# Kernel tuning notes

Hardware: AMD Instinct MI355X
Metric: run time of the kernel (lower is better)

Reference implementation:

```python
import jax, jax.numpy as jnp
import numpy as np
from jax import lax

NH = 8        # num_heads
C = 256       # embedding_dim
WS = 5        # window_size
DN = ('NCHW', 'OIHW', 'NCHW')


def setup_inputs() -> dict:
    key = jax.random.key(0)
    ks = jax.random.split(key, 6)
    B, H, W = 16, 64, 64
    hd = C // NH  # per-head dim = pos_embed_dim
    return {
        "src": jax.random.normal(ks[0], (B, C, H, W), jnp.float32),
        "rel_pos_embed": jax.random.normal(ks[1], (hd, WS, WS), jnp.float32) * 0.02,
        "qkv_w": jax.random.normal(ks[2], (3 * C, C), jnp.float32) * (C ** -0.5),
        "cpe_w": jax.random.normal(ks[3], (C, C, 3, 3), jnp.float32) * (1.0 / np.sqrt(C * 9)),
        "cpe_b": jnp.zeros((C,), jnp.float32),
        "out_w": jax.random.normal(ks[4], (C, C), jnp.float32) * (C ** -0.5),
        "out_b": jnp.zeros((C,), jnp.float32),
    }


def reference(src, rel_pos_embed, qkv_w, cpe_w, cpe_b, out_w, out_b):
    B, Cc, H, W = src.shape
    hd = Cc // NH
    scale = hd ** -0.5

    # conv positional encoding (3x3 conv) + residual
    x = lax.conv_general_dilated(src, cpe_w, (1, 1), [(1, 1), (1, 1)],
                                 dimension_numbers=DN) + cpe_b[None, :, None, None] + src

    # 1x1 qkv conv as a GEMM over channels
    qkv = jnp.einsum('oc,bchw->bohw', qkv_w, x)
    q, k, v = jnp.split(qkv, 3, axis=1)
    q = q.reshape(B * NH, hd, H, W)
    k = k.reshape(B * NH, hd, H, W)
    v = v.reshape(B * NH, hd, H, W)

    # linear (lambda) attention: softmax over spatial positions of k
    kf = jax.nn.softmax(k.reshape(B * NH, hd, H * W), axis=-1)   # (b' i n)
    vf = v.reshape(B * NH, hd, H * W)                            # (b' o n)
    content_lambda = jnp.einsum('bin,bon->bio', kf, vf)          # (b' i o), tiny
    qf = q.reshape(B * NH, hd, H * W) * scale
    content = jnp.einsum('bin,bio->bon', qf, content_lambda).reshape(B * NH, hd, H, W)

    # depthwise conv positional lambda on v
    pad = WS // 2
    pos_lambda = lax.conv_general_dilated(v, rel_pos_embed[:, None], (1, 1),
                                          [(pad, pad), (pad, pad)],
                                          dimension_numbers=DN,
                                          feature_group_count=hd)
    result = (content + q * pos_lambda).reshape(B, Cc, H, W)

    # 1x1 output projection
    return jnp.einsum('oc,bchw->bohw', out_w, result) + out_b[None, :, None, None]
```

## Files before the change

### kernel.cpp

```cpp
#include <hip/hip_runtime.h>


typedef unsigned short u16;
typedef __bf16 bf16x8 __attribute__((ext_vector_type(8)));
typedef float f32x4 __attribute__((ext_vector_type(4)));
#define HW 4096

__device__ __forceinline__ float bf2f(u16 u){
  unsigned v = ((unsigned)u) << 16;
  return __builtin_bit_cast(float, v);
}
__device__ __forceinline__ u16 f2bf(float f){
  unsigned u = __builtin_bit_cast(unsigned, f);
  u = u + 0x7fffu + ((u >> 16) & 1u);
  return (u16)(u >> 16);
}
__device__ __forceinline__ unsigned pack2(float a, float b){
  return (unsigned)f2bf(a) | ((unsigned)f2bf(b) << 16);
}
__device__ __forceinline__ void unpack2(unsigned u, float& a, float& b){
  a = bf2f((u16)(u & 0xffffu)); b = bf2f((u16)(u >> 16));
}
__device__ __forceinline__ void unp8(uint4 r, float* v){
  unpack2(r.x, v[0], v[1]); unpack2(r.y, v[2], v[3]);
  unpack2(r.z, v[4], v[5]); unpack2(r.w, v[6], v[7]);
}

__device__ __forceinline__ void gl2lds16(const u16* g, u16* l){
  __builtin_amdgcn_global_load_lds((__attribute__((address_space(1))) void*)g,
                                   (__attribute__((address_space(3))) void*)l, 16, 0, 0);
}

__global__ void zero_border(u16* __restrict__ xpad){
  int idx = blockIdx.x*256 + threadIdx.x;
  int g = idx & 31;
  int p = idx >> 5;
  int b = p / 260; int r = p - b*260;
  int y, x;
  if (r < 66)      { y = 0;      x = r; }
  else if (r < 132){ y = 65;     x = r-66; }
  else if (r < 196){ y = r-131;  x = 0; }
  else             { y = r-195;  x = 65; }
  *(uint4*)&xpad[((size_t)b*4356 + (size_t)y*66 + x)*256 + g*8] = uint4{0,0,0,0};
}

__global__ __launch_bounds__(256) void to_nhwc(const float* __restrict__ src,
                                               u16* __restrict__ xpad){
  __shared__ u16 sl[64*264];
  const int t = threadIdx.x, w = t>>6, lane = t&63;
  const int y = blockIdx.x, b = blockIdx.y;
  for (int cc = 0; cc < 64; ++cc){
    const int c = cc*4 + w;
    float v = src[((size_t)(b*256 + c))*HW + y*64 + lane];
    sl[lane*264 + c] = f2bf(v);
  }
  __syncthreads();
  #pragma unroll
  for (int i = 0; i < 8; ++i){
    int idx = t + 256*i;
    int p = idx >> 5, g = idx & 31;
    uint4 v = *(const uint4*)&sl[p*264 + g*8];
    *(uint4*)&xpad[((size_t)b*4356 + (size_t)(y+1)*66 + (p+1))*256 + g*8] = v;
  }
}

__global__ void repack_w(const float* __restrict__ cpe_w, const float* __restrict__ qkv_w,
                         const float* __restrict__ out_w, u16* __restrict__ wrb,
                         u16* __restrict__ wq, u16* __restrict__ wo){
  int idx = blockIdx.x*256 + threadIdx.x;
  if (idx < 589824){
    int kk = idx >> 16, o = (idx >> 8) & 255, c = idx & 255;
    wrb[idx] = f2bf(cpe_w[((o*256 + c)*9) + kk]);
  } else if (idx < 786432){
    int j = idx - 589824;
    wq[j] = f2bf(qkv_w[j]);
  } else {
    int j = idx - 786432;
    wo[j] = f2bf(out_w[j]);
  }
}

__global__ __launch_bounds__(256) void conv_mfma(const u16* __restrict__ xpad,
    const u16* __restrict__ wrb, const float* __restrict__ bias,
    u16* __restrict__ xout){
  __shared__ u16 As[8192];
  __shared__ u16 Bs[8192];
  const int t = threadIdx.x, w = t>>6, lane = t&63;
  const int idx = blockIdx.x;
  const int x8 = idx&7, q = idx>>3;
  const int ot = q & 1, nb = (q>>1)*8 + x8;
  const int pg = nb*128;
  const int b = pg>>12, hw0 = pg&4095, y0 = hw0>>6;
  const int o0 = ot*128;
  const size_t xb = (size_t)b*4356;
  const int sp8 = t>>3;
  const int cs8 = (t&7) ^ (sp8&7);
  const u16* aA[4]; const u16* bB[4];
  #pragma unroll
  for (int i = 0; i < 4; ++i){
    aA[i] = xpad + (xb + (size_t)(y0 + (i>>1) + 1)*66 + ((i&1)*32 + sp8) + 1)*256 + cs8*8;
    bB[i] = wrb + (size_t)(o0 + i*32 + sp8)*256 + cs8*8;
  }
  const int wm = w&1, wn = w>>1;
  const int qd = lane>>4;
  int a_off[4], b_off[4];
  #pragma unroll
  for (int i = 0; i < 4; ++i){
    int p = wm*64 + i*16 + (lane&15);
    a_off[i] = p*64 + ((qd ^ (p&7)) << 3);
    int r = wn*64 + i*16 + (lane&15);
    b_off[i] = r*64 + ((qd ^ (r&7)) << 3);
  }
  f32x4 acc[4][4];
  #pragma unroll
  for (int i=0;i<4;++i)
    #pragma unroll
    for (int j=0;j<4;++j) acc[i][j] = f32x4{0.f,0.f,0.f,0.f};

  for (int c0 = 0; c0 < 256; c0 += 64){
    for (int kk = 0; kk < 9; ++kk){
      const int toff = ((kk/3 - 1)*66 + (kk%3 - 1))*256 + c0;
      const int woff = kk*65536 + c0;
      __syncthreads();
      #pragma unroll
      for (int i = 0; i < 4; ++i){
        gl2lds16(aA[i] + toff, &As[i*2048 + t*8]);
        gl2lds16(bB[i] + woff, &Bs[i*2048 + t*8]);
      }
      __syncthreads();
      #pragma unroll
      for (int kh = 0; kh < 2; ++kh){
        bf16x8 af[4], bfr[4];
        #pragma unroll
        for (int i = 0; i < 4; ++i){
          af[i]  = __builtin_bit_cast(bf16x8, *(const uint4*)&As[a_off[i] ^ (kh<<5)]);
          bfr[i] = __builtin_bit_cast(bf16x8, *(const uint4*)&Bs[b_off[i] ^ (kh<<5)]);
        }
        #pragma unroll
        for (int mt = 0; mt < 4; ++mt)
          #pragma unroll
          for (int nt = 0; nt < 4; ++nt)
            acc[mt][nt] = __builtin_amdgcn_mfma_f32_16x16x32_bf16(bfr[nt], af[mt], acc[mt][nt], 0,0,0);
      }
    }
  }
  #pragma unroll
  for (int nt = 0; nt < 4; ++nt){
    const int och4 = o0 + wn*64 + nt*16 + (lane>>4)*4;
    float4 b4 = *(const float4*)&bias[och4];
    #pragma unroll
    for (int mt = 0; mt < 4; ++mt){
      const int px = wm*64 + mt*16 + (lane&15);
      const int hw = hw0 + px;
      const int y = hw>>6, x = hw&63;
      ushort4 r4 = *(const ushort4*)&xpad[(xb + (size_t)(y+1)*66 + x + 1)*256 + och4];
      ushort4 s;
      s.x = f2bf(acc[mt][nt][0] + b4.x + bf2f(r4.x));
      s.y = f2bf(acc[mt][nt][1] + b4.y + bf2f(r4.y));
      s.z = f2bf(acc[mt][nt][2] + b4.z + bf2f(r4.z));
      s.w = f2bf(acc[mt][nt][3] + b4.w + bf2f(r4.w));
      *(ushort4*)&xout[(size_t)(pg + px)*256 + och4] = s;
    }
  }
}

template<int NO, int NOT, bool F32OUT>
__global__ __launch_bounds__(256) void gemm_mfma(const u16* __restrict__ act,
    const u16* __restrict__ wt, const float* __restrict__ bias, void* __restrict__ out){
  __shared__ u16 As[8192];
  __shared__ u16 Bs[8192];
  const int t = threadIdx.x, w = t>>6, lane = t&63;
  const int idx = blockIdx.x;
  const int x8 = idx&7, q = idx>>3;
  const int ot = q % NOT, nb = (q / NOT)*8 + x8;
  const int pg = nb*128, o0 = ot*128;
  const int sp8 = t>>3;
  const int cs8 = (t&7) ^ (sp8&7);
  const u16* aA[4]; const u16* bB[4];
  #pragma unroll
  for (int i = 0; i < 4; ++i){
    aA[i] = act + (size_t)(pg + i*32 + sp8)*256 + cs8*8;
    bB[i] = wt  + (size_t)(o0 + i*32 + sp8)*256 + cs8*8;
  }
  const int wm = w&1, wn = w>>1;
  const int qd = lane>>4;
  int a_off[4], b_off[4];
  #pragma unroll
  for (int i = 0; i < 4; ++i){
    int p = wm*64 + i*16 + (lane&15);
    a_off[i] = p*64 + ((qd ^ (p&7)) << 3);
    int r = wn*64 + i*16 + (lane&15);
    b_off[i] = r*64 + ((qd ^ (r&7)) << 3);
  }
  f32x4 acc[4][4];
  #pragma unroll
  for (int i=0;i<4;++i)
    #pragma unroll
    for (int j=0;j<4;++j) acc[i][j] = f32x4{0.f,0.f,0.f,0.f};

  for (int c0 = 0; c0 < 256; c0 += 64){
    __syncthreads();
    #pragma unroll
    for (int i = 0; i < 4; ++i){
      gl2lds16(aA[i] + c0, &As[i*2048 + t*8]);
      gl2lds16(bB[i] + c0, &Bs[i*2048 + t*8]);
    }
    __syncthreads();
    #pragma unroll
    for (int kh = 0; kh < 2; ++kh){
      bf16x8 af[4], bfr[4];
      #pragma unroll
      for (int i = 0; i < 4; ++i){
        af[i]  = __builtin_bit_cast(bf16x8, *(const uint4*)&As[a_off[i] ^ (kh<<5)]);
        bfr[i] = __builtin_bit_cast(bf16x8, *(const uint4*)&Bs[b_off[i] ^ (kh<<5)]);
      }
      #pragma unroll
      for (int mt = 0; mt < 4; ++mt)
        #pragma unroll
        for (int nt = 0; nt < 4; ++nt){
          if constexpr (F32OUT)
            acc[mt][nt] = __builtin_amdgcn_mfma_f32_16x16x32_bf16(af[mt], bfr[nt], acc[mt][nt], 0,0,0);
          else
            acc[mt][nt] = __builtin_amdgcn_mfma_f32_16x16x32_bf16(bfr[nt], af[mt], acc[mt][nt], 0,0,0);
        }
    }
  }
  if constexpr (F32OUT){
    const int col = lane&15, row_l = (lane>>4)*4;
    const int b = pg>>12, hw0 = pg&4095;
    float* op = (float*)out;
    #pragma unroll
    for (int nt = 0; nt < 4; ++nt){
      const int och = o0 + wn*64 + nt*16 + col;
      const float bo = bias[och];
      #pragma unroll
      for (int mt = 0; mt < 4; ++mt){
        const int pl = wm*64 + mt*16 + row_l;
        float4 v;
        v.x = acc[mt][nt][0]+bo; v.y = acc[mt][nt][1]+bo;
        v.z = acc[mt][nt][2]+bo; v.w = acc[mt][nt][3]+bo;
        *(float4*)&op[((size_t)b*256 + och)*HW + hw0 + pl] = v;
      }
    }
  } else {
    u16* op = (u16*)out;
    #pragma unroll
    for (int nt = 0; nt < 4; ++nt){
      const int och4 = o0 + wn*64 + nt*16 + (lane>>4)*4;
      #pragma unroll
      for (int mt = 0; mt < 4; ++mt){
        const int px = wm*64 + mt*16 + (lane&15);
        ushort4 s;
        s.x = f2bf(acc[mt][nt][0]); s.y = f2bf(acc[mt][nt][1]);
        s.z = f2bf(acc[mt][nt][2]); s.w = f2bf(acc[mt][nt][3]);
        *(ushort4*)&op[(size_t)(pg + px)*NO + och4] = s;
      }
    }
  }
}

__global__ void zero_cl(float* __restrict__ cl){
  cl[blockIdx.x*256 + threadIdx.x] = 0.f;
}

__global__ __launch_bounds__(64) void lambda_kern(const u16* __restrict__ qkv,
                                                  float* __restrict__ cl,
                                                  float* __restrict__ S){
  __shared__ float Kl[64*36];
  __shared__ float Vl[64*36];
  const int t = threadIdx.x;
  const int bp = blockIdx.x, split = blockIdx.y;
  const int b = bp>>3, h = bp&7;
  const int ig = t&7, og = t>>3;
  float acc[4][4];
  float sacc[4] = {0.f,0.f,0.f,0.f};
  #pragma unroll
  for (int i=0;i<4;++i)
    #pragma unroll
    for (int j=0;j<4;++j) acc[i][j] = 0.f;
  for (int chunk = 0; chunk < 8; ++chunk){
    const int n = split*512 + chunk*64 + t;
    const u16* kp = qkv + (size_t)(b*HW + n)*768 + 256 + h*32;
    const u16* vp = kp + 256;
    uint4 k4[4], v4[4];
    #pragma unroll
    for (int qq=0;qq<4;++qq){ k4[qq] = ((const uint4*)kp)[qq]; v4[qq] = ((const uint4*)vp)[qq]; }
    __syncthreads();
    #pragma unroll
    for (int qq=0;qq<4;++qq){
      float kv[8], vv[8]; unp8(k4[qq], kv); unp8(v4[qq], vv);
      #pragma unroll
      for (int e=0;e<8;++e) kv[e] = __expf(kv[e]);
      *(float4*)&Kl[t*36 + qq*8]     = float4{kv[0],kv[1],kv[2],kv[3]};
      *(float4*)&Kl[t*36 + qq*8 + 4] = float4{kv[4],kv[5],kv[6],kv[7]};
      *(float4*)&Vl[t*36 + qq*8]     = float4{vv[0],vv[1],vv[2],vv[3]};
      *(float4*)&Vl[t*36 + qq*8 + 4] = float4{vv[4],vv[5],vv[6],vv[7]};
    }
    __syncthreads();
    for (int p = 0; p < 64; ++p){
      float4 kf = *(const float4*)&Kl[p*36 + ig*4];
      float4 vf = *(const float4*)&Vl[p*36 + og*4];
      float kfa[4] = {kf.x,kf.y,kf.z,kf.w};
      float vfa[4] = {vf.x,vf.y,vf.z,vf.w};
      #pragma unroll
      for (int i=0;i<4;++i){
        sacc[i] += kfa[i];
        #pragma unroll
        for (int j=0;j<4;++j) acc[i][j] = fmaf(kfa[i], vfa[j], acc[i][j]);
      }
    }
  }
  #pragma unroll
  for (int i=0;i<4;++i)
    #pragma unroll
    for (int j=0;j<4;++j)
      atomicAdd(&cl[(size_t)bp*1024 + (ig*4+i)*32 + og*4+j], acc[i][j]);
  if (og == 0){
    #pragma unroll
    for (int i=0;i<4;++i) atomicAdd(&S[bp*32 + ig*4 + i], sacc[i]);
  }
}

__global__ __launch_bounds__(256) void content_combine(const u16* __restrict__ qkv,
    const float* __restrict__ cl, const float* __restrict__ S,
    const float* __restrict__ rel, u16* __restrict__ res){
  __shared__ u16 vt[12800];
  __shared__ float relT[800];
  const int t = threadIdx.x;
  const int tile = blockIdx.x, h = blockIdx.y, b = blockIdx.z;
  const int x0 = (tile&3)*16, y0 = (tile>>2)*16;
  const float* __restrict__ clp = cl + (size_t)(b*8+h)*1024;
  const float* __restrict__ Sp  = S + (b*8+h)*32;
  for (int idx = t; idx < 800; idx += 256){
    int tap = idx>>5, ch = idx&31;
    relT[idx] = rel[ch*25 + tap];
  }
  #pragma unroll
  for (int i = 0; i < 7; ++i){
    int idx = t + 256*i;
    if (idx < 1600){
      int hp = idx>>2, g = idx&3;
      int hy = hp/20, hx = hp - hy*20;
      int y = y0 + hy - 2, x = x0 + hx - 2;
      uint4 v = uint4{0,0,0,0};
      if ((unsigned)y < 64u && (unsigned)x < 64u)
        v = *(const uint4*)&qkv[(size_t)(b*HW + y*64 + x)*768 + 512 + h*32 + g*8];
      *(uint4*)&vt[hp*32 + ((g ^ (hx&3))<<3)] = v;
    }
  }
  __syncthreads();
  const int py = t>>4, px = t&15;
  const int pix = b*HW + (y0+py)*64 + x0 + px;
  const u16* qp = qkv + (size_t)pix*768 + h*32;
  float qv[32];
  {
    uint4 q0 = ((const uint4*)qp)[0], q1 = ((const uint4*)qp)[1];
    uint4 q2 = ((const uint4*)qp)[2], q3 = ((const uint4*)qp)[3];
    unp8(q0, qv); unp8(q1, qv+8); unp8(q2, qv+16); unp8(q3, qv+24);
  }
  float outv[32];
  #pragma unroll
  for (int j=0;j<32;++j) outv[j] = 0.f;
  for (int i = 0; i < 32; ++i){
    const float qi = qv[i] * 0.17677669529663687f * __builtin_amdgcn_rcpf(Sp[i]);
    #pragma unroll
    for (int g = 0; g < 8; ++g){
      float4 c4 = *(const float4*)&clp[i*32 + g*4];
      outv[g*4+0] = fmaf(qi, c4.x, outv[g*4+0]);
      outv[g*4+1] = fmaf(qi, c4.y, outv[g*4+1]);
      outv[g*4+2] = fmaf(qi, c4.z, outv[g*4+2]);
      outv[g*4+3] = fmaf(qi, c4.w, outv[g*4+3]);
    }
  }
  #pragma unroll
  for (int chg = 0; chg < 4; ++chg){
    float pos[8];
    #pragma unroll
    for (int j=0;j<8;++j) pos[j] = 0.f;
    #pragma unroll
    for (int dy = 0; dy < 5; ++dy)
      #pragma unroll
      for (int dx = 0; dx < 5; ++dx){
        int hx = px + dx;
        uint4 v4 = *(const uint4*)&vt[((py+dy)*20 + hx)*32 + ((chg ^ (hx&3))<<3)];
        float vv[8]; unp8(v4, vv);
        float4 r0 = *(const float4*)&relT[(dy*5+dx)*32 + chg*8];
        float4 r1 = *(const float4*)&relT[(dy*5+dx)*32 + chg*8 + 4];
        pos[0]=fmaf(r0.x, vv[0], pos[0]); pos[1]=fmaf(r0.y, vv[1], pos[1]);
        pos[2]=fmaf(r0.z, vv[2], pos[2]); pos[3]=fmaf(r0.w, vv[3], pos[3]);
        pos[4]=fmaf(r1.x, vv[4], pos[4]); pos[5]=fmaf(r1.y, vv[5], pos[5]);
        pos[6]=fmaf(r1.z, vv[6], pos[6]); pos[7]=fmaf(r1.w, vv[7], pos[7]);
      }
    #pragma unroll
    for (int j=0;j<8;++j) outv[chg*8+j] = fmaf(qv[chg*8+j], pos[j], outv[chg*8+j]);
  }
  u16* rp = res + (size_t)pix*256 + h*32;
  #pragma unroll
  for (int g = 0; g < 4; ++g){
    uint4 o_;
    o_.x = pack2(outv[g*8+0], outv[g*8+1]);
    o_.y = pack2(outv[g*8+2], outv[g*8+3]);
    o_.z = pack2(outv[g*8+4], outv[g*8+5]);
    o_.w = pack2(outv[g*8+6], outv[g*8+7]);
    ((uint4*)rp)[g] = o_;
  }
}

extern "C" void kernel_launch(void* const* d_in, const int* in_sizes, int n_in,
                              void* d_out, int out_size, void* d_ws, size_t ws_size,
                              hipStream_t stream) {
  const float* src   = (const float*)d_in[0];
  const float* rel   = (const float*)d_in[1];
  const float* qkv_w = (const float*)d_in[2];
  const float* cpe_w = (const float*)d_in[3];
  const float* cpe_b = (const float*)d_in[4];
  const float* out_w = (const float*)d_in[5];
  const float* out_b = (const float*)d_in[6];
  char* ws = (char*)d_ws;
  u16*   qkv  = (u16*)(ws);
  u16*   xpad = (u16*)(ws);
  u16*   xbuf = (u16*)(ws + 100663296);
  float* cl   = (float*)(ws + 134217728);
  float* S    = (float*)(ws + 134742016);
  u16*   wrb  = (u16*)(ws + 134758400);
  u16*   wq   = (u16*)(ws + 135938048);
  u16*   wo   = (u16*)(ws + 136331264);

  zero_border<<<dim3(520), dim3(256), 0, stream>>>(xpad);
  to_nhwc<<<dim3(64, 16), dim3(256), 0, stream>>>(src, xpad);
  repack_w<<<dim3(3328), dim3(256), 0, stream>>>(cpe_w, qkv_w, out_w, wrb, wq, wo);
  conv_mfma<<<dim3(1024), dim3(256), 0, stream>>>(xpad, wrb, cpe_b, xbuf);
  gemm_mfma<768,6,false><<<dim3(3072), dim3(256), 0, stream>>>(xbuf, wq, nullptr, (void*)qkv);
  zero_cl<<<dim3(528), dim3(256), 0, stream>>>(cl);
  lambda_kern<<<dim3(128, 8), dim3(64), 0, stream>>>(qkv, cl, S);
  content_combine<<<dim3(16, 8, 16), dim3(256), 0, stream>>>(qkv, cl, S, rel, xbuf);
  gemm_mfma<256,2,true><<<dim3(1024), dim3(256), 0, stream>>>(xbuf, wo, out_b, d_out);
}
```

Baseline: 459.6 us.

## Double-buffer LDS tiles in conv and GEMM MFMA kernels to overlap loads

Both the 3x3 conv kernel and the 1x1 GEMM kernel now use two LDS buffers. The global-to-LDS copies for the next k-step are issued before the MFMAs on the current buffer, with a partial vmcnt wait plus barrier in place of two full __syncthreads per step. This hides global load latency behind compute. The cost is twice the shared memory (64 KB per block), which may lower occupancy, and it relies on hand-written waitcnt counts being correct.

After: 451.1 us. No clear change (-1.9%).

```diff
diff --git a/kernel.cpp b/kernel.cpp
--- a/kernel.cpp
+++ b/kernel.cpp
@@ -83,8 +83,8 @@
 __global__ __launch_bounds__(256) void conv_mfma(const u16* __restrict__ xpad,
     const u16* __restrict__ wrb, const float* __restrict__ bias,
     u16* __restrict__ xout){
-  __shared__ u16 As[8192];
-  __shared__ u16 Bs[8192];
+  __shared__ u16 As[16384];
+  __shared__ u16 Bs[16384];
   const int t = threadIdx.x, w = t>>6, lane = t&63;
   const int idx = blockIdx.x;
   const int x8 = idx&7, q = idx>>3;
@@ -117,32 +117,48 @@
     #pragma unroll
     for (int j=0;j<4;++j) acc[i][j] = f32x4{0.f,0.f,0.f,0.f};
 
-  for (int c0 = 0; c0 < 256; c0 += 64){
-    for (int kk = 0; kk < 9; ++kk){
-      const int toff = ((kk/3 - 1)*66 + (kk%3 - 1))*256 + c0;
-      const int woff = kk*65536 + c0;
-      __syncthreads();
+  int ky = 0, kx = 0, c0 = 0;
+  {
+    const int to = ((ky-1)*66 + (kx-1))*256 + c0;
+    const int wo = (ky*3+kx)*65536 + c0;
+    #pragma unroll
+    for (int i = 0; i < 4; ++i){
+      gl2lds16(aA[i] + to, &As[i*2048 + t*8]);
+      gl2lds16(bB[i] + wo, &Bs[i*2048 + t*8]);
+    }
+    ++kx;
+  }
+  for (int s = 0; s < 36; ++s){
+    const int bo = (s&1)*8192;
+    if (s < 35){
+      const int nbo = ((s+1)&1)*8192;
+      const int to = ((ky-1)*66 + (kx-1))*256 + c0;
+      const int wo = (ky*3+kx)*65536 + c0;
       #pragma unroll
       for (int i = 0; i < 4; ++i){
-        gl2lds16(aA[i] + toff, &As[i*2048 + t*8]);
-        gl2lds16(bB[i] + woff, &Bs[i*2048 + t*8]);
-      }
-      __syncthreads();
-      #pragma unroll
-      for (int kh = 0; kh < 2; ++kh){
-        bf16x8 af[4], bfr[4];
+        gl2lds16(aA[i] + to, &As[nbo + i*2048 + t*8]);
+        gl2lds16(bB[i] + wo, &Bs[nbo + i*2048 + t*8]);
+      }
+      ++kx; if (kx==3){ kx=0; ++ky; if (ky==3){ ky=0; c0 += 64; } }
+      asm volatile("s_waitcnt vmcnt(8)\n\ts_barrier" ::: "memory");
+    } else {
+      asm volatile("s_waitcnt vmcnt(0)\n\ts_barrier" ::: "memory");
+    }
+    #pragma unroll
+    for (int kh = 0; kh < 2; ++kh){
+      bf16x8 af[4], bfr[4];
+      #pragma unroll
+      for (int i = 0; i < 4; ++i){
+        af[i]  = __builtin_bit_cast(bf16x8, *(const uint4*)&As[bo + (a_off[i] ^ (kh<<5))]);
+        bfr[i] = __builtin_bit_cast(bf16x8, *(const uint4*)&Bs[bo + (b_off[i] ^ (kh<<5))]);
+      }
+      #pragma unroll
+      for (int mt = 0; mt < 4; ++mt)
         #pragma unroll
-        for (int i = 0; i < 4; ++i){
-          af[i]  = __builtin_bit_cast(bf16x8, *(const uint4*)&As[a_off[i] ^ (kh<<5)]);
-          bfr[i] = __builtin_bit_cast(bf16x8, *(const uint4*)&Bs[b_off[i] ^ (kh<<5)]);
-        }
-        #pragma unroll
-        for (int mt = 0; mt < 4; ++mt)
-          #pragma unroll
-          for (int nt = 0; nt < 4; ++nt)
-            acc[mt][nt] = __builtin_amdgcn_mfma_f32_16x16x32_bf16(bfr[nt], af[mt], acc[mt][nt], 0,0,0);
-      }
-    }
+        for (int nt = 0; nt < 4; ++nt)
+          acc[mt][nt] = __builtin_amdgcn_mfma_f32_16x16x32_bf16(bfr[nt], af[mt], acc[mt][nt], 0,0,0);
+    }
+    if (s < 35) asm volatile("s_barrier" ::: "memory");
   }
   #pragma unroll
   for (int nt = 0; nt < 4; ++nt){
@@ -167,8 +183,8 @@
 template<int NO, int NOT, bool F32OUT>
 __global__ __launch_bounds__(256) void gemm_mfma(const u16* __restrict__ act,
     const u16* __restrict__ wt, const float* __restrict__ bias, void* __restrict__ out){
-  __shared__ u16 As[8192];
-  __shared__ u16 Bs[8192];
+  __shared__ u16 As[16384];
+  __shared__ u16 Bs[16384];
   const int t = threadIdx.x, w = t>>6, lane = t&63;
   const int idx = blockIdx.x;
   const int x8 = idx&7, q = idx>>3;
@@ -198,21 +214,32 @@
     #pragma unroll
     for (int j=0;j<4;++j) acc[i][j] = f32x4{0.f,0.f,0.f,0.f};
 
-  for (int c0 = 0; c0 < 256; c0 += 64){
-    __syncthreads();
-    #pragma unroll
-    for (int i = 0; i < 4; ++i){
-      gl2lds16(aA[i] + c0, &As[i*2048 + t*8]);
-      gl2lds16(bB[i] + c0, &Bs[i*2048 + t*8]);
-    }
-    __syncthreads();
+  #pragma unroll
+  for (int i = 0; i < 4; ++i){
+    gl2lds16(aA[i], &As[i*2048 + t*8]);
+    gl2lds16(bB[i], &Bs[i*2048 + t*8]);
+  }
+  for (int s = 0; s < 4; ++s){
+    const int bo = (s&1)*8192;
+    if (s < 3){
+      const int nbo = ((s+1)&1)*8192;
+      const int cn = (s+1)*64;
+      #pragma unroll
+      for (int i = 0; i < 4; ++i){
+        gl2lds16(aA[i] + cn, &As[nbo + i*2048 + t*8]);
+        gl2lds16(bB[i] + cn, &Bs[nbo + i*2048 + t*8]);
+      }
+      asm volatile("s_waitcnt vmcnt(8)\n\ts_barrier" ::: "memory");
+    } else {
+      asm volatile("s_waitcnt vmcnt(0)\n\ts_barrier" ::: "memory");
+    }
     #pragma unroll
     for (int kh = 0; kh < 2; ++kh){
       bf16x8 af[4], bfr[4];
       #pragma unroll
       for (int i = 0; i < 4; ++i){
-        af[i]  = __builtin_bit_cast(bf16x8, *(const uint4*)&As[a_off[i] ^ (kh<<5)]);
-        bfr[i] = __builtin_bit_cast(bf16x8, *(const uint4*)&Bs[b_off[i] ^ (kh<<5)]);
+        af[i]  = __builtin_bit_cast(bf16x8, *(const uint4*)&As[bo + (a_off[i] ^ (kh<<5))]);
+        bfr[i] = __builtin_bit_cast(bf16x8, *(const uint4*)&Bs[bo + (b_off[i] ^ (kh<<5))]);
       }
       #pragma unroll
       for (int mt = 0; mt < 4; ++mt)
@@ -224,6 +251,7 @@
             acc[mt][nt] = __builtin_amdgcn_mfma_f32_16x16x32_bf16(bfr[nt], af[mt], acc[mt][nt], 0,0,0);
         }
     }
+    if (s < 3) asm volatile("s_barrier" ::: "memory");
   }
   if constexpr (F32OUT){
     const int col = lane&15, row_l = (lane>>4)*4;
@@ -232,13 +260,13 @@
     #pragma unroll
     for (int nt = 0; nt < 4; ++nt){
       const int och = o0 + wn*64 + nt*16 + col;
-      const float bo = bias[och];
+      const float bo2 = bias[och];
       #pragma unroll
       for (int mt = 0; mt < 4; ++mt){
         const int pl = wm*64 + mt*16 + row_l;
         float4 v;
-        v.x = acc[mt][nt][0]+bo; v.y = acc[mt][nt][1]+bo;
-        v.z = acc[mt][nt][2]+bo; v.w = acc[mt][nt][3]+bo;
+        v.x = acc[mt][nt][0]+bo2; v.y = acc[mt][nt][1]+bo2;
+        v.z = acc[mt][nt][2]+bo2; v.w = acc[mt][nt][3]+bo2;
         *(float4*)&op[((size_t)b*256 + och)*HW + hw0 + pl] = v;
       }
     }
```

## Use 256x256 double-buffered MFMA tiles with 512 threads for conv and GEMMs

Applied to the files above, without the earlier changes.

The 3x3 conv and both 1x1 GEMM kernels move from 128x128 tiles with 256 threads to 256x256 tiles with 512 threads, each wave computing 128x64. LDS is double-buffered so the next K-chunk's global-to-LDS copy overlaps the MFMA work on the current one. Waits use raw vmcnt and barrier, and MFMA sections run at raised priority. Grids shrink to 256/768/256 blocks, which raises operand reuse per block but uses about 128KB of LDS per block and leaves fewer blocks to hide latency.

Result: faster. 436.7 us (-5.0%).

```diff
diff --git a/kernel.cpp b/kernel.cpp
--- a/kernel.cpp
+++ b/kernel.cpp
@@ -80,79 +80,94 @@
   }
 }
 
-__global__ __launch_bounds__(256) void conv_mfma(const u16* __restrict__ xpad,
+__global__ __launch_bounds__(512, 2) void conv_mfma(const u16* __restrict__ xpad,
     const u16* __restrict__ wrb, const float* __restrict__ bias,
     u16* __restrict__ xout){
-  __shared__ u16 As[8192];
-  __shared__ u16 Bs[8192];
-  const int t = threadIdx.x, w = t>>6, lane = t&63;
+  __shared__ u16 As[32768];
+  __shared__ u16 Bs[32768];
+  const int t = threadIdx.x, w8 = t>>6, lane = t&63;
   const int idx = blockIdx.x;
-  const int x8 = idx&7, q = idx>>3;
-  const int ot = q & 1, nb = (q>>1)*8 + x8;
-  const int pg = nb*128;
-  const int b = pg>>12, hw0 = pg&4095, y0 = hw0>>6;
-  const int o0 = ot*128;
+  const int nb = (idx&7)*32 + (idx>>3);
+  const int pg = nb*256;
+  const int b = pg>>12, row0 = (pg&4095)>>6;
   const size_t xb = (size_t)b*4356;
-  const int sp8 = t>>3;
-  const int cs8 = (t&7) ^ (sp8&7);
-  const u16* aA[4]; const u16* bB[4];
+  const int dstb = w8*2048 + lane*8;
+  const u16* aP[4]; const u16* bP[4];
   #pragma unroll
   for (int i = 0; i < 4; ++i){
-    aA[i] = xpad + (xb + (size_t)(y0 + (i>>1) + 1)*66 + ((i&1)*32 + sp8) + 1)*256 + cs8*8;
-    bB[i] = wrb + (size_t)(o0 + i*32 + sp8)*256 + cs8*8;
-  }
-  const int wm = w&1, wn = w>>1;
+    int G = (w8*4+i)*64 + lane;
+    int p = G>>3, gs = (G&7) ^ (p&7);
+    aP[i] = xpad + (xb + (size_t)(row0 + (p>>6) + 1)*66 + (p&63) + 1)*256 + gs*8;
+    bP[i] = wrb + (size_t)p*256 + gs*8;
+  }
+  const int wm = w8>>2, wn = w8&3;
   const int qd = lane>>4;
-  int a_off[4], b_off[4];
-  #pragma unroll
-  for (int i = 0; i < 4; ++i){
-    int p = wm*64 + i*16 + (lane&15);
-    a_off[i] = p*64 + ((qd ^ (p&7)) << 3);
-    int r = wn*64 + i*16 + (lane&15);
-    b_off[i] = r*64 + ((qd ^ (r&7)) << 3);
-  }
-  f32x4 acc[4][4];
-  #pragma unroll
-  for (int i=0;i<4;++i)
+  int a_off[8], b_off[4];
+  #pragma unroll
+  for (int m = 0; m < 8; ++m){
+    int p = wm*128 + m*16 + (lane&15);
+    a_off[m] = p*64 + ((qd ^ (p&7)) << 3);
+  }
+  #pragma unroll
+  for (int n = 0; n < 4; ++n){
+    int r = wn*64 + n*16 + (lane&15);
+    b_off[n] = r*64 + ((qd ^ (r&7)) << 3);
+  }
+  f32x4 acc[8][4];
+  #pragma unroll
+  for (int i=0;i<8;++i)
     #pragma unroll
     for (int j=0;j<4;++j) acc[i][j] = f32x4{0.f,0.f,0.f,0.f};
 
-  for (int c0 = 0; c0 < 256; c0 += 64){
-    for (int kk = 0; kk < 9; ++kk){
-      const int toff = ((kk/3 - 1)*66 + (kk%3 - 1))*256 + c0;
-      const int woff = kk*65536 + c0;
-      __syncthreads();
-      #pragma unroll
-      for (int i = 0; i < 4; ++i){
-        gl2lds16(aA[i] + toff, &As[i*2048 + t*8]);
-        gl2lds16(bB[i] + woff, &Bs[i*2048 + t*8]);
-      }
-      __syncthreads();
-      #pragma unroll
-      for (int kh = 0; kh < 2; ++kh){
-        bf16x8 af[4], bfr[4];
+  auto STAGE = [&](const int bufo, const int s){
+    int c9 = s/9, tap = s - c9*9, ky = tap/3, kx = tap - ky*3;
+    int offA = ((ky-1)*66 + (kx-1))*256 + c9*64;
+    int offB = tap*65536 + c9*64;
+    #pragma unroll
+    for (int i = 0; i < 4; ++i){
+      gl2lds16(aP[i] + offA, &As[bufo + dstb + i*512]);
+      gl2lds16(bP[i] + offB, &Bs[bufo + dstb + i*512]);
+    }
+  };
+  auto COMPUTE = [&](const int bufo){
+    __builtin_amdgcn_s_setprio(1);
+    #pragma unroll
+    for (int kh = 0; kh < 2; ++kh){
+      bf16x8 af[8], bfr[4];
+      #pragma unroll
+      for (int m = 0; m < 8; ++m)
+        af[m] = __builtin_bit_cast(bf16x8, *(const uint4*)&As[bufo + (a_off[m] ^ (kh<<5))]);
+      #pragma unroll
+      for (int n = 0; n < 4; ++n)
+        bfr[n] = __builtin_bit_cast(bf16x8, *(const uint4*)&Bs[bufo + (b_off[n] ^ (kh<<5))]);
+      #pragma unroll
+      for (int mt = 0; mt < 8; ++mt)
         #pragma unroll
-        for (int i = 0; i < 4; ++i){
-          af[i]  = __builtin_bit_cast(bf16x8, *(const uint4*)&As[a_off[i] ^ (kh<<5)]);
-          bfr[i] = __builtin_bit_cast(bf16x8, *(const uint4*)&Bs[b_off[i] ^ (kh<<5)]);
-        }
-        #pragma unroll
-        for (int mt = 0; mt < 4; ++mt)
-          #pragma unroll
-          for (int nt = 0; nt < 4; ++nt)
-            acc[mt][nt] = __builtin_amdgcn_mfma_f32_16x16x32_bf16(bfr[nt], af[mt], acc[mt][nt], 0,0,0);
-      }
-    }
+        for (int nt = 0; nt < 4; ++nt)
+          acc[mt][nt] = __builtin_amdgcn_mfma_f32_16x16x32_bf16(bfr[nt], af[mt], acc[mt][nt], 0,0,0);
+    }
+    __builtin_amdgcn_s_setprio(0);
+  };
+  #define SYNC asm volatile("s_waitcnt vmcnt(0)" ::: "memory"); __builtin_amdgcn_s_barrier();
+
+  STAGE(0, 0);
+  SYNC
+  for (int s2 = 0; s2 < 18; ++s2){
+    STAGE(16384, 2*s2+1);
+    COMPUTE(0);
+    SYNC
+    if (s2 < 17) STAGE(0, 2*s2+2);
+    COMPUTE(16384);
+    SYNC
   }
   #pragma unroll
   for (int nt = 0; nt < 4; ++nt){
-    const int och4 = o0 + wn*64 + nt*16 + (lane>>4)*4;
+    const int och4 = wn*64 + nt*16 + qd*4;
     float4 b4 = *(const float4*)&bias[och4];
     #pragma unroll
-    for (int mt = 0; mt < 4; ++mt){
-      const int px = wm*64 + mt*16 + (lane&15);
-      const int hw = hw0 + px;
-      const int y = hw>>6, x = hw&63;
+    for (int mt = 0; mt < 8; ++mt){
+      const int px = wm*128 + mt*16 + (lane&15);
+      const int y = row0 + (px>>6), x = px&63;
       ushort4 r4 = *(const ushort4*)&xpad[(xb + (size_t)(y+1)*66 + x + 1)*256 + och4];
       ushort4 s;
       s.x = f2bf(acc[mt][nt][0] + b4.x + bf2f(r4.x));
@@ -162,60 +177,68 @@
       *(ushort4*)&xout[(size_t)(pg + px)*256 + och4] = s;
     }
   }
+  #undef SYNC
 }
 
 template<int NO, int NOT, bool F32OUT>
-__global__ __launch_bounds__(256) void gemm_mfma(const u16* __restrict__ act,
+__global__ __launch_bounds__(512, 2) void gemm_mfma(const u16* __restrict__ act,
     const u16* __restrict__ wt, const float* __restrict__ bias, void* __restrict__ out){
-  __shared__ u16 As[8192];
-  __shared__ u16 Bs[8192];
-  const int t = threadIdx.x, w = t>>6, lane = t&63;
+  __shared__ u16 As[32768];
+  __shared__ u16 Bs[32768];
+  const int t = threadIdx.x, w8 = t>>6, lane = t&63;
   const int idx = blockIdx.x;
   const int x8 = idx&7, q = idx>>3;
-  const int ot = q % NOT, nb = (q / NOT)*8 + x8;
-  const int pg = nb*128, o0 = ot*128;
-  const int sp8 = t>>3;
-  const int cs8 = (t&7) ^ (sp8&7);
-  const u16* aA[4]; const u16* bB[4];
+  const int ot = q % NOT, nb = x8*32 + q / NOT;
+  const int pg = nb*256, o0 = ot*256;
+  const int dstb = w8*2048 + lane*8;
+  const u16* aP[4]; const u16* bP[4];
   #pragma unroll
   for (int i = 0; i < 4; ++i){
-    aA[i] = act + (size_t)(pg + i*32 + sp8)*256 + cs8*8;
-    bB[i] = wt  + (size_t)(o0 + i*32 + sp8)*256 + cs8*8;
-  }
-  const int wm = w&1, wn = w>>1;
+    int G = (w8*4+i)*64 + lane;
+    int p = G>>3, gs = (G&7) ^ (p&7);
+    aP[i] = act + (size_t)(pg + p)*256 + gs*8;
+    bP[i] = wt  + (size_t)(o0 + p)*256 + gs*8;
+  }
+  const int wm = w8>>2, wn = w8&3;
   const int qd = lane>>4;
-  int a_off[4], b_off[4];
-  #pragma unroll
-  for (int i = 0; i < 4; ++i){
-    int p = wm*64 + i*16 + (lane&15);
-    a_off[i] = p*64 + ((qd ^ (p&7)) << 3);
-    int r = wn*64 + i*16 + (lane&15);
-    b_off[i] = r*64 + ((qd ^ (r&7)) << 3);
-  }
-  f32x4 acc[4][4];
-  #pragma unroll
-  for (int i=0;i<4;++i)
+  int a_off[8], b_off[4];
+  #pragma unroll
+  for (int m = 0; m < 8; ++m){
+    int p = wm*128 + m*16 + (lane&15);
+    a_off[m] = p*64 + ((qd ^ (p&7)) << 3);
+  }
+  #pragma unroll
+  for (int n = 0; n < 4; ++n){
+    int r = wn*64 + n*16 + (lane&15);
+    b_off[n] = r*64 + ((qd ^ (r&7)) << 3);
+  }
+  f32x4 acc[8][4];
+  #pragma unroll
+  for (int i=0;i<8;++i)
     #pragma unroll
     for (int j=0;j<4;++j) acc[i][j] = f32x4{0.f,0.f,0.f,0.f};
 
-  for (int c0 = 0; c0 < 256; c0 += 64){
-    __syncthreads();
+  auto STAGE = [&](const int bufo, const int s){
+    const int c0 = s*64;
     #pragma unroll
     for (int i = 0; i < 4; ++i){
-      gl2lds16(aA[i] + c0, &As[i*2048 + t*8]);
-      gl2lds16(bB[i] + c0, &Bs[i*2048 + t*8]);
-    }
-    __syncthreads();
+      gl2lds16(aP[i] + c0, &As[bufo + dstb + i*512]);
+      gl2lds16(bP[i] + c0, &Bs[bufo + dstb + i*512]);
+    }
+  };
+  auto COMPUTE = [&](const int bufo){
+    __builtin_amdgcn_s_setprio(1);
     #pragma unroll
     for (int kh = 0; kh < 2; ++kh){
-      bf16x8 af[4], bfr[4];
-      #pragma unroll
-      for (int i = 0; i < 4; ++i){
-        af[i]  = __builtin_bit_cast(bf16x8, *(const uint4*)&As[a_off[i] ^ (kh<<5)]);
-        bfr[i] = __builtin_bit_cast(bf16x8, *(const uint4*)&Bs[b_off[i] ^ (kh<<5)]);
-      }
-      #pragma unroll
-      for (int mt = 0; mt < 4; ++mt)
+      bf16x8 af[8], bfr[4];
+      #pragma unroll
+      for (int m = 0; m < 8; ++m)
+        af[m] = __builtin_bit_cast(bf16x8, *(const uint4*)&As[bufo + (a_off[m] ^ (kh<<5))]);
+      #pragma unroll
+      for (int n = 0; n < 4; ++n)
+        bfr[n] = __builtin_bit_cast(bf16x8, *(const uint4*)&Bs[bufo + (b_off[n] ^ (kh<<5))]);
+      #pragma unroll
+      for (int mt = 0; mt < 8; ++mt)
         #pragma unroll
         for (int nt = 0; nt < 4; ++nt){
           if constexpr (F32OUT)
@@ -224,21 +247,34 @@
             acc[mt][nt] = __builtin_amdgcn_mfma_f32_16x16x32_bf16(bfr[nt], af[mt], acc[mt][nt], 0,0,0);
         }
     }
+    __builtin_amdgcn_s_setprio(0);
+  };
+  #define SYNC asm volatile("s_waitcnt vmcnt(0)" ::: "memory"); __builtin_amdgcn_s_barrier();
+
+  STAGE(0, 0);
+  SYNC
+  for (int s2 = 0; s2 < 2; ++s2){
+    STAGE(16384, 2*s2+1);
+    COMPUTE(0);
+    SYNC
+    if (s2 < 1) STAGE(0, 2*s2+2);
+    COMPUTE(16384);
+    SYNC
   }
   if constexpr (F32OUT){
-    const int col = lane&15, row_l = (lane>>4)*4;
+    const int col = lane&15, row_l = qd*4;
     const int b = pg>>12, hw0 = pg&4095;
     float* op = (float*)out;
     #pragma unroll
     for (int nt = 0; nt < 4; ++nt){
       const int och = o0 + wn*64 + nt*16 + col;
-      const float bo = bias[och];
-      #pragma unroll
-      for (int mt = 0; mt < 4; ++mt){
-        const int pl = wm*64 + mt*16 + row_l;
+      const float bo2 = bias[och];
+      #pragma unroll
+      for (int mt = 0; mt < 8; ++mt){
+        const int pl = wm*128 + mt*16 + row_l;
         float4 v;
-        v.x = acc[mt][nt][0]+bo; v.y = acc[mt][nt][1]+bo;
-        v.z = acc[mt][nt][2]+bo; v.w = acc[mt][nt][3]+bo;
+        v.x = acc[mt][nt][0]+bo2; v.y = acc[mt][nt][1]+bo2;
+        v.z = acc[mt][nt][2]+bo2; v.w = acc[mt][nt][3]+bo2;
         *(float4*)&op[((size_t)b*256 + och)*HW + hw0 + pl] = v;
       }
     }
@@ -246,10 +282,10 @@
     u16* op = (u16*)out;
     #pragma unroll
     for (int nt = 0; nt < 4; ++nt){
-      const int och4 = o0 + wn*64 + nt*16 + (lane>>4)*4;
-      #pragma unroll
-      for (int mt = 0; mt < 4; ++mt){
-        const int px = wm*64 + mt*16 + (lane&15);
+      const int och4 = o0 + wn*64 + nt*16 + qd*4;
+      #pragma unroll
+      for (int mt = 0; mt < 8; ++mt){
+        const int px = wm*128 + mt*16 + (lane&15);
         ushort4 s;
         s.x = f2bf(acc[mt][nt][0]); s.y = f2bf(acc[mt][nt][1]);
         s.z = f2bf(acc[mt][nt][2]); s.w = f2bf(acc[mt][nt][3]);
@@ -257,6 +293,7 @@
       }
     }
   }
+  #undef SYNC
 }
 
 __global__ void zero_cl(float* __restrict__ cl){
@@ -429,10 +466,10 @@
   zero_border<<<dim3(520), dim3(256), 0, stream>>>(xpad);
   to_nhwc<<<dim3(64, 16), dim3(256), 0, stream>>>(src, xpad);
   repack_w<<<dim3(3328), dim3(256), 0, stream>>>(cpe_w, qkv_w, out_w, wrb, wq, wo);
-  conv_mfma<<<dim3(1024), dim3(256), 0, stream>>>(xpad, wrb, cpe_b, xbuf);
-  gemm_mfma<768,6,false><<<dim3(3072), dim3(256), 0, stream>>>(xbuf, wq, nullptr, (void*)qkv);
+  conv_mfma<<<dim3(256), dim3(512), 0, stream>>>(xpad, wrb, cpe_b, xbuf);
+  gemm_mfma<768,3,false><<<dim3(768), dim3(512), 0, stream>>>(xbuf, wq, nullptr, (void*)qkv);
   zero_cl<<<dim3(528), dim3(256), 0, stream>>>(cl);
   lambda_kern<<<dim3(128, 8), dim3(64), 0, stream>>>(qkv, cl, S);
   content_combine<<<dim3(16, 8, 16), dim3(256), 0, stream>>>(qkv, cl, S, rel, xbuf);
-  gemm_mfma<256,2,true><<<dim3(1024), dim3(256), 0, stream>>>(xbuf, wo, out_b, d_out);
-}
+  gemm_mfma<256,1,true><<<dim3(256), dim3(512), 0, stream>>>(xbuf, wo, out_b, d_out);
+}
```
